# Kernel tuning notes

Hardware: AMD Instinct MI355X
Metric: run time of the kernel (lower is better)

Reference implementation:

```python
import jax, jax.numpy as jnp
import numpy as np

B, N, E, H, HID = 4, 2048, 1024, 16, 4096
D = E // H
EPS = 1e-5


def setup_inputs() -> dict:
    key = jax.random.key(0)
    ks = jax.random.split(key, 8)
    s = 0.02
    return {
        "x": jax.random.normal(ks[0], (B, N, E), dtype=jnp.float32),
        "Wqkv": jax.random.normal(ks[1], (3 * E, E), dtype=jnp.float32) * s,
        "bqkv": jnp.zeros((3 * E,), dtype=jnp.float32),
        "Wo": jax.random.normal(ks[2], (E, E), dtype=jnp.float32) * s,
        "bo": jnp.zeros((E,), dtype=jnp.float32),
        "ln1_g": jnp.ones((E,), dtype=jnp.float32),
        "ln1_b": jnp.zeros((E,), dtype=jnp.float32),
        "W1": jax.random.normal(ks[3], (HID, E), dtype=jnp.float32) * s,
        "bf1": jnp.zeros((HID,), dtype=jnp.float32),
        "W2": jax.random.normal(ks[4], (E, HID), dtype=jnp.float32) * s,
        "bf2": jnp.zeros((E,), dtype=jnp.float32),
        "ln2_g": jnp.ones((E,), dtype=jnp.float32),
        "ln2_b": jnp.zeros((E,), dtype=jnp.float32),
    }


def _layernorm(x, g, b):
    m = jnp.mean(x, axis=-1, keepdims=True)
    v = jnp.mean(jnp.square(x - m), axis=-1, keepdims=True)
    return (x - m) * jax.lax.rsqrt(v + EPS) * g + b


def reference(x, Wqkv, bqkv, Wo, bo, ln1_g, ln1_b, W1, bf1, W2, bf2, ln2_g, ln2_b):
    Bx, Nx, Ex = x.shape
    # --- MultiHeadSelfAttention (faithful to original, including its einsum-label quirk) ---
    qkv = x @ Wqkv.T + bqkv                                   # (B,N,3E)
    qkv = qkv.reshape(Bx, Nx, 3, H, D).transpose(2, 0, 3, 1, 4)  # (3,B,H,N,D)
    q, k, v = qkv[0], qkv[1], qkv[2]                          # each (B,H,N,D)
    # original torch labels: q/k interpreted as (n,q,h,d) -> energy (B,N,H,H)
    energy = jnp.einsum('nqhd,nkhd->nhqk', q, k)
    attention = jax.nn.softmax(energy / (Ex ** 0.5), axis=-1)  # softmax over heads axis
    out = jnp.einsum('nhql,nlhd->nqhd', attention, v).reshape(Bx, Nx, Ex)
    attn_out = out @ Wo.T + bo
    # --- residual + LN1 ---
    h = _layernorm(x + attn_out, ln1_g, ln1_b)
    # --- FFN (dropout is identity in eval) ---
    f = jax.nn.gelu(h @ W1.T + bf1, approximate=False) @ W2.T + bf2
    # --- residual + LN2 ---
    return _layernorm(h + f, ln2_g, ln2_b)
```

## Files before the change

### kernel.cpp

```cpp
#include <hip/hip_runtime.h>
#include <hip/hip_bf16.h>
#include <math.h>

typedef __hip_bfloat16 bf16;
typedef __bf16 bf8v __attribute__((ext_vector_type(8)));
typedef float f4v __attribute__((ext_vector_type(4)));

__device__ inline float gelu_act(float v) {
    return 0.5f * v * (1.f + erff(v * 0.70710678118654752f));
}

__device__ inline void gld16(const void* g, void* l) {
    __builtin_amdgcn_global_load_lds(
        (__attribute__((address_space(1))) void*)g,
        (__attribute__((address_space(3))) void*)l, 16, 0, 0);
}

__global__ __launch_bounds__(256)
void cast_f2b(const float* __restrict__ X, bf16* __restrict__ Y, long n)
{
    const long i = ((long)blockIdx.x * 256 + threadIdx.x) * 4;
    if (i + 3 < n) {
        const float4 v = *(const float4*)(X + i);
        Y[i + 0] = __float2bfloat16(v.x);
        Y[i + 1] = __float2bfloat16(v.y);
        Y[i + 2] = __float2bfloat16(v.z);
        Y[i + 3] = __float2bfloat16(v.w);
    }
}

template<int EPI, bool HASRES, typename CT, int KL, int KR>
__global__ __launch_bounds__(256, 4)
void gemm128(const bf16* __restrict__ A, const bf16* __restrict__ W,
             const float* __restrict__ bias, const float* __restrict__ Rr,
             CT* __restrict__ C, int N)
{
    extern __shared__ __align__(16) unsigned short lds[];
    constexpr int NT   = KL / 32;
    constexpr int SLOT = 8192;

    const int o     = blockIdx.y * gridDim.x + blockIdx.x;
    const int local = o >> 3;
    const int bm  = (o & 7) * 8 + (local & 7);
    const int bn  = local >> 3;
    const long row0 = (long)bm * 128;
    const long col0 = (long)bn * 128;
    const long koff = (long)blockIdx.z * KL;

    const int tid  = threadIdx.x;
    const int lane = tid & 63;
    const int wave = tid >> 6;
    const int wm = wave >> 1;
    const int wn = wave & 1;
    const int fr = lane & 15;
    const int q4 = (lane >> 4) * 4;
    const int ksw = (((lane >> 4) ^ ((lane >> 1) & 3)) << 3);

    const int srow = tid >> 2;
    const int csrc = (tid & 3) ^ ((srow >> 1) & 3);
    const unsigned short* gA = (const unsigned short*)A + (row0 + srow) * (long)KR + koff + csrc * 8;
    const unsigned short* gB = (const unsigned short*)W + (col0 + srow) * (long)KR + koff + csrc * 8;
    const int woff = wave * 512;

    auto stage = [&](int t) {
        const long k0 = (long)t * 32;
        unsigned short* sl = lds + (t & 1) * SLOT + woff;
        gld16(gA + k0,                  sl);
        gld16(gA + 64 * (long)KR + k0,  sl + 2048);
        gld16(gB + k0,                  sl + 4096);
        gld16(gB + 64 * (long)KR + k0,  sl + 6144);
    };

    f4v acc[4][4];
#pragma unroll
    for (int i = 0; i < 4; ++i)
#pragma unroll
        for (int j = 0; j < 4; ++j) acc[i][j] = {0.f, 0.f, 0.f, 0.f};

    stage(0);
    __syncthreads();

#pragma unroll 2
    for (int t = 0; t < NT; ++t) {
        if (t + 1 < NT) stage(t + 1);

        const unsigned short* sA = lds + (t & 1) * SLOT;
        const unsigned short* sB = sA + 4096;

        bf8v afrag[4], bfrag[4];
#pragma unroll
        for (int x = 0; x < 4; ++x) {
            afrag[x] = *(const bf8v*)&sA[(wm * 64 + x * 16 + fr) * 32 + ksw];
            bfrag[x] = *(const bf8v*)&sB[(wn * 64 + x * 16 + fr) * 32 + ksw];
        }
#pragma unroll
        for (int mi = 0; mi < 4; ++mi)
#pragma unroll
            for (int ni = 0; ni < 4; ++ni)
                acc[mi][ni] = __builtin_amdgcn_mfma_f32_16x16x32_bf16(
                    afrag[mi], bfrag[ni], acc[mi][ni], 0, 0, 0);

        __syncthreads();
    }

    if constexpr (EPI == 2) {
        const bool addb = (blockIdx.z == 0);
#pragma unroll
        for (int ni = 0; ni < 4; ++ni) {
            const long n = col0 + wn * 64 + ni * 16 + fr;
            const float bvv = addb ? bias[n] : 0.f;
#pragma unroll
            for (int mi = 0; mi < 4; ++mi) {
                const long mb = row0 + wm * 64 + mi * 16 + q4;
#pragma unroll
                for (int r = 0; r < 4; ++r)
                    atomicAdd((float*)&C[(mb + r) * (long)N + n], acc[mi][ni][r] + bvv);
            }
        }
        return;
    }

    constexpr int STR = 132;
    float* eb = (float*)lds;
    const int lcol  = (tid & 31) * 4;
    const long nbase = col0 + lcol;
    const float4 b4 = *(const float4*)&bias[nbase];
    const float bb[4] = {b4.x, b4.y, b4.z, b4.w};

#pragma unroll
    for (int h = 0; h < 2; ++h) {
        if (h) __syncthreads();
        if (wm == h) {
#pragma unroll
            for (int mi = 0; mi < 4; ++mi)
#pragma unroll
                for (int ni = 0; ni < 4; ++ni)
#pragma unroll
                    for (int r = 0; r < 4; ++r)
                        eb[(mi * 16 + q4 + r) * STR + wn * 64 + ni * 16 + fr] = acc[mi][ni][r];
        }
        __syncthreads();
#pragma unroll
        for (int i = 0; i < 8; ++i) {
            const int  rh = i * 8 + (tid >> 5);
            const long gr = row0 + h * 64 + rh;
            const f4v v = *(const f4v*)&eb[rh * STR + lcol];
            float ov[4];
#pragma unroll
            for (int c = 0; c < 4; ++c) ov[c] = v[c] + bb[c];
            if (HASRES) {
                const float4 r4 = *(const float4*)&Rr[gr * (long)N + nbase];
                const float ra[4] = {r4.x, r4.y, r4.z, r4.w};
#pragma unroll
                for (int c = 0; c < 4; ++c) ov[c] += ra[c];
            }
            if (EPI == 1) {
#pragma unroll
                for (int c = 0; c < 4; ++c) ov[c] = gelu_act(ov[c]);
            }
            if constexpr (sizeof(CT) == 2) {
                ushort4 s;
                bf16* sp = (bf16*)&s;
#pragma unroll
                for (int c = 0; c < 4; ++c) sp[c] = __float2bfloat16(ov[c]);
                *(ushort4*)&C[gr * (long)N + nbase] = s;
            } else {
                *(float4*)&C[gr * (long)N + nbase] = make_float4(ov[0], ov[1], ov[2], ov[3]);
            }
        }
    }
}

__global__ __launch_bounds__(256)
void attn_kernel(const bf16* __restrict__ qkv, bf16* __restrict__ scr)
{
    __shared__ float sb[4][3392];
    const int tid = threadIdx.x;
    const int wave = tid >> 6, lane = tid & 63;
    const int m = blockIdx.x * 4 + wave;

    float* q = sb[wave];
    float* k = q + 1040;
    float* v = k + 1040;
    float* a = v + 1040;

    const bf16* rowp = qkv + (size_t)m * 3072;
    for (int i = lane; i < 1024; i += 64) {
        int hh = i >> 6, dd = i & 63;
        q[hh * 65 + dd] = __bfloat162float(rowp[i]);
        k[hh * 65 + dd] = __bfloat162float(rowp[1024 + i]);
        v[hh * 65 + dd] = __bfloat162float(rowp[2048 + i]);
    }
    __syncthreads();

    const int h1 = lane & 15, qd = lane >> 4;
    float e[4];
#pragma unroll
    for (int j = 0; j < 4; ++j) {
        const float* qr = q + h1 * 65;
        const float* kr = k + (qd * 4 + j) * 65;
        float s0 = 0.f;
        for (int d = 0; d < 64; ++d) s0 += qr[d] * kr[d];
        e[j] = s0 * 0.03125f;
    }
    float mx = fmaxf(fmaxf(e[0], e[1]), fmaxf(e[2], e[3]));
    mx = fmaxf(mx, __shfl_xor(mx, 16, 64));
    mx = fmaxf(mx, __shfl_xor(mx, 32, 64));
    float p[4], ps = 0.f;
#pragma unroll
    for (int j = 0; j < 4; ++j) { p[j] = expf(e[j] - mx); ps += p[j]; }
    ps += __shfl_xor(ps, 16, 64);
    ps += __shfl_xor(ps, 32, 64);
    const float inv = 1.f / ps;
#pragma unroll
    for (int j = 0; j < 4; ++j) a[h1 * 17 + qd * 4 + j] = p[j] * inv;
    __syncthreads();

    const int h = lane & 15, dg = lane >> 4;
    float arow[16];
#pragma unroll
    for (int l2 = 0; l2 < 16; ++l2) arow[l2] = a[h * 17 + l2];
    const int b = m >> 11, j = m & 2047;
    bf16* op = scr + (((size_t)b * 2048 + h * 128 + (j >> 4)) * 1024 + (j & 15) * 64);
    for (int t = 0; t < 16; ++t) {
        const int d = dg * 16 + t;
        float o = 0.f;
#pragma unroll
        for (int l2 = 0; l2 < 16; ++l2) o += arow[l2] * v[l2 * 65 + d];
        op[d] = __float2bfloat16(o);
    }
}

__global__ __launch_bounds__(256)
void ln_kernel(const float* __restrict__ X, const float* __restrict__ G,
               const float* __restrict__ Bt, float* __restrict__ Y32,
               bf16* __restrict__ Yb)
{
    __shared__ float rs[4], rq[4];
    const int tid = threadIdx.x;
    const long row = blockIdx.x;
    const float* xp = X + row * 1024;
    float x[4];
#pragma unroll
    for (int i = 0; i < 4; ++i) x[i] = xp[tid + 256 * i];

    float s = x[0] + x[1] + x[2] + x[3];
#pragma unroll
    for (int off = 32; off; off >>= 1) s += __shfl_down(s, off, 64);
    if ((tid & 63) == 0) rs[tid >> 6] = s;
    __syncthreads();
    const float mean = (rs[0] + rs[1] + rs[2] + rs[3]) * (1.f / 1024.f);

    float qv = 0.f;
#pragma unroll
    for (int i = 0; i < 4; ++i) { float d = x[i] - mean; qv += d * d; }
#pragma unroll
    for (int off = 32; off; off >>= 1) qv += __shfl_down(qv, off, 64);
    if ((tid & 63) == 0) rq[tid >> 6] = qv;
    __syncthreads();
    const float var = (rq[0] + rq[1] + rq[2] + rq[3]) * (1.f / 1024.f);
    const float rstd = rsqrtf(var + 1e-5f);

#pragma unroll
    for (int i = 0; i < 4; ++i) {
        const int e = tid + 256 * i;
        const float yv = (x[i] - mean) * rstd * G[e] + Bt[e];
        Y32[row * 1024 + e] = yv;
        if (Yb) Yb[row * 1024 + e] = __float2bfloat16(yv);
    }
}

extern "C" void kernel_launch(void* const* d_in, const int* in_sizes, int n_in,
                              void* d_out, int out_size, void* d_ws, size_t ws_size,
                              hipStream_t stream)
{
    (void)in_sizes; (void)n_in; (void)out_size;
    const float* x    = (const float*)d_in[0];
    const float* Wqkv = (const float*)d_in[1];
    const float* bqkv = (const float*)d_in[2];
    const float* Wo   = (const float*)d_in[3];
    const float* bo   = (const float*)d_in[4];
    const float* g1   = (const float*)d_in[5];
    const float* b1   = (const float*)d_in[6];
    const float* W1   = (const float*)d_in[7];
    const float* bf1  = (const float*)d_in[8];
    const float* W2   = (const float*)d_in[9];
    const float* bf2  = (const float*)d_in[10];
    const float* g2   = (const float*)d_in[11];
    const float* b2   = (const float*)d_in[12];
    float* out = (float*)d_out;

    if (ws_size < 125829120ULL) return;

    char* ws = (char*)d_ws;
    bf16* qkv   = (bf16*)(ws + 0);
    float* t    = (float*)(ws + 0);
    bf16* u     = (bf16*)(ws + 0);
    bf16* Wqkvb = (bf16*)(ws + 67108864);
    bf16* Wob   = (bf16*)(ws + 73400320);
    bf16* W1b   = (bf16*)(ws + 75497472);
    bf16* W2b   = (bf16*)(ws + 83886080);
    bf16* xb    = (bf16*)(ws + 92274688);
    bf16* scr   = (bf16*)(ws + 92274688);
    bf16* hb    = (bf16*)(ws + 109051904);
    float* h    = out;

    constexpr unsigned LDS_128 = 33792;
    constexpr unsigned LDS_SPK = 32768;

    cast_f2b<<<8192, 256, 0, stream>>>(x,    xb,    8388608);
    cast_f2b<<<3072, 256, 0, stream>>>(Wqkv, Wqkvb, 3145728);
    cast_f2b<<<1024, 256, 0, stream>>>(Wo,   Wob,   1048576);
    cast_f2b<<<4096, 256, 0, stream>>>(W1,   W1b,   4194304);
    cast_f2b<<<4096, 256, 0, stream>>>(W2,   W2b,   4194304);

    gemm128<0, false, bf16, 1024, 1024><<<dim3(64, 24), 256, LDS_128, stream>>>(xb, Wqkvb, bqkv, nullptr, qkv, 3072);
    attn_kernel<<<2048, 256, 0, stream>>>(qkv, scr);
    gemm128<0, true, float, 1024, 1024><<<dim3(64, 8), 256, LDS_128, stream>>>(scr, Wob, bo, x, t, 1024);
    ln_kernel<<<8192, 256, 0, stream>>>(t, g1, b1, h, hb);
    gemm128<1, false, bf16, 1024, 1024><<<dim3(64, 32), 256, LDS_128, stream>>>(hb, W1b, bf1, nullptr, u, 4096);
    gemm128<2, false, float, 2048, 4096><<<dim3(64, 8, 2), 256, LDS_SPK, stream>>>(u, W2b, bf2, nullptr, out, 1024);
    ln_kernel<<<8192, 256, 0, stream>>>(out, g2, b2, out, nullptr);
}
```

Before: 493.9 us.

## Fuse weight casts, vectorize attention I/O, drop split-K atomics in FFN2

Merges the five fp32-to-bf16 cast launches into one kernel that writes packed 4-element bf16 stores. The attention kernel now loads q/k/v rows with 16-byte vector loads and writes its output with 16-byte vector stores instead of scalar bf16 accesses. The second FFN GEMM becomes a single full-K GEMM whose epilogue adds the residual h, in place of a two-way split-K with per-element float atomicAdd. This removes atomic traffic and redundant launches, but halves the block count of the largest GEMM, which lowers parallelism, and the residual is read from the same buffer the result is written to.

```diff
diff --git a/kernel.cpp b/kernel.cpp
--- a/kernel.cpp
+++ b/kernel.cpp
@@ -5,9 +5,18 @@
 typedef __hip_bfloat16 bf16;
 typedef __bf16 bf8v __attribute__((ext_vector_type(8)));
 typedef float f4v __attribute__((ext_vector_type(4)));
+typedef unsigned short u16x8 __attribute__((ext_vector_type(8)));
+typedef unsigned short u16x4 __attribute__((ext_vector_type(4)));
 
 __device__ inline float gelu_act(float v) {
     return 0.5f * v * (1.f + erff(v * 0.70710678118654752f));
+}
+__device__ inline float b2f(unsigned short u) {
+    return __uint_as_float((unsigned)u << 16);
+}
+__device__ inline unsigned short f2b(float f) {
+    bf16 b = __float2bfloat16(f);
+    return *reinterpret_cast<unsigned short*>(&b);
 }
 
 __device__ inline void gld16(const void* g, void* l) {
@@ -17,16 +26,24 @@
 }
 
 __global__ __launch_bounds__(256)
-void cast_f2b(const float* __restrict__ X, bf16* __restrict__ Y, long n)
-{
-    const long i = ((long)blockIdx.x * 256 + threadIdx.x) * 4;
-    if (i + 3 < n) {
-        const float4 v = *(const float4*)(X + i);
-        Y[i + 0] = __float2bfloat16(v.x);
-        Y[i + 1] = __float2bfloat16(v.y);
-        Y[i + 2] = __float2bfloat16(v.z);
-        Y[i + 3] = __float2bfloat16(v.w);
-    }
+void cast_all(const float* __restrict__ x, const float* __restrict__ Wqkv,
+              const float* __restrict__ Wo, const float* __restrict__ W1,
+              const float* __restrict__ W2, bf16* __restrict__ xb,
+              bf16* __restrict__ Wqkvb, bf16* __restrict__ Wob,
+              bf16* __restrict__ W1b, bf16* __restrict__ W2b)
+{
+    const int b = blockIdx.x;
+    const float* src; bf16* dst; long off;
+    if (b < 8192)       { src = x;    dst = xb;    off = b; }
+    else if (b < 11264) { src = Wqkv; dst = Wqkvb; off = b - 8192; }
+    else if (b < 12288) { src = Wo;   dst = Wob;   off = b - 11264; }
+    else if (b < 16384) { src = W1;   dst = W1b;   off = b - 12288; }
+    else                { src = W2;   dst = W2b;   off = b - 16384; }
+    const long i = (off * 256 + threadIdx.x) * 4;
+    const float4 v = *(const float4*)(src + i);
+    u16x4 s;
+    s[0] = f2b(v.x); s[1] = f2b(v.y); s[2] = f2b(v.z); s[3] = f2b(v.w);
+    *(u16x4*)((unsigned short*)dst + i) = s;
 }
 
 template<int EPI, bool HASRES, typename CT, int KL, int KR>
@@ -103,23 +120,6 @@
         __syncthreads();
     }
 
-    if constexpr (EPI == 2) {
-        const bool addb = (blockIdx.z == 0);
-#pragma unroll
-        for (int ni = 0; ni < 4; ++ni) {
-            const long n = col0 + wn * 64 + ni * 16 + fr;
-            const float bvv = addb ? bias[n] : 0.f;
-#pragma unroll
-            for (int mi = 0; mi < 4; ++mi) {
-                const long mb = row0 + wm * 64 + mi * 16 + q4;
-#pragma unroll
-                for (int r = 0; r < 4; ++r)
-                    atomicAdd((float*)&C[(mb + r) * (long)N + n], acc[mi][ni][r] + bvv);
-            }
-        }
-        return;
-    }
-
     constexpr int STR = 132;
     float* eb = (float*)lds;
     const int lcol  = (tid & 31) * 4;
@@ -184,12 +184,24 @@
     float* v = k + 1040;
     float* a = v + 1040;
 
-    const bf16* rowp = qkv + (size_t)m * 3072;
-    for (int i = lane; i < 1024; i += 64) {
-        int hh = i >> 6, dd = i & 63;
-        q[hh * 65 + dd] = __bfloat162float(rowp[i]);
-        k[hh * 65 + dd] = __bfloat162float(rowp[1024 + i]);
-        v[hh * 65 + dd] = __bfloat162float(rowp[2048 + i]);
+    {
+        const unsigned short* rp = (const unsigned short*)(qkv + (size_t)m * 3072) + lane * 16;
+        const int hh = lane >> 2, dd = (lane & 3) * 16;
+        const u16x8 a0 = *(const u16x8*)(rp);
+        const u16x8 a1 = *(const u16x8*)(rp + 8);
+        const u16x8 b0 = *(const u16x8*)(rp + 1024);
+        const u16x8 b1 = *(const u16x8*)(rp + 1032);
+        const u16x8 c0 = *(const u16x8*)(rp + 2048);
+        const u16x8 c1 = *(const u16x8*)(rp + 2056);
+        float* qdst = q + hh * 65 + dd;
+        float* kdst = k + hh * 65 + dd;
+        float* vdst = v + hh * 65 + dd;
+#pragma unroll
+        for (int j = 0; j < 8; ++j) {
+            qdst[j] = b2f(a0[j]); qdst[8 + j] = b2f(a1[j]);
+            kdst[j] = b2f(b0[j]); kdst[8 + j] = b2f(b1[j]);
+            vdst[j] = b2f(c0[j]); vdst[8 + j] = b2f(c1[j]);
+        }
     }
     __syncthreads();
 
@@ -222,13 +234,20 @@
     for (int l2 = 0; l2 < 16; ++l2) arow[l2] = a[h * 17 + l2];
     const int b = m >> 11, j = m & 2047;
     bf16* op = scr + (((size_t)b * 2048 + h * 128 + (j >> 4)) * 1024 + (j & 15) * 64);
+
+    float ov[16];
+#pragma unroll
     for (int t = 0; t < 16; ++t) {
-        const int d = dg * 16 + t;
         float o = 0.f;
 #pragma unroll
-        for (int l2 = 0; l2 < 16; ++l2) o += arow[l2] * v[l2 * 65 + d];
-        op[d] = __float2bfloat16(o);
-    }
+        for (int l2 = 0; l2 < 16; ++l2) o += arow[l2] * v[l2 * 65 + dg * 16 + t];
+        ov[t] = o;
+    }
+    u16x8 s0, s1;
+#pragma unroll
+    for (int jj = 0; jj < 8; ++jj) { s0[jj] = f2b(ov[jj]); s1[jj] = f2b(ov[8 + jj]); }
+    *(u16x8*)((unsigned short*)op + dg * 16)     = s0;
+    *(u16x8*)((unsigned short*)op + dg * 16 + 8) = s1;
 }
 
 __global__ __launch_bounds__(256)
@@ -306,19 +325,14 @@
     float* h    = out;
 
     constexpr unsigned LDS_128 = 33792;
-    constexpr unsigned LDS_SPK = 32768;
-
-    cast_f2b<<<8192, 256, 0, stream>>>(x,    xb,    8388608);
-    cast_f2b<<<3072, 256, 0, stream>>>(Wqkv, Wqkvb, 3145728);
-    cast_f2b<<<1024, 256, 0, stream>>>(Wo,   Wob,   1048576);
-    cast_f2b<<<4096, 256, 0, stream>>>(W1,   W1b,   4194304);
-    cast_f2b<<<4096, 256, 0, stream>>>(W2,   W2b,   4194304);
+
+    cast_all<<<20480, 256, 0, stream>>>(x, Wqkv, Wo, W1, W2, xb, Wqkvb, Wob, W1b, W2b);
 
     gemm128<0, false, bf16, 1024, 1024><<<dim3(64, 24), 256, LDS_128, stream>>>(xb, Wqkvb, bqkv, nullptr, qkv, 3072);
     attn_kernel<<<2048, 256, 0, stream>>>(qkv, scr);
     gemm128<0, true, float, 1024, 1024><<<dim3(64, 8), 256, LDS_128, stream>>>(scr, Wob, bo, x, t, 1024);
     ln_kernel<<<8192, 256, 0, stream>>>(t, g1, b1, h, hb);
     gemm128<1, false, bf16, 1024, 1024><<<dim3(64, 32), 256, LDS_128, stream>>>(hb, W1b, bf1, nullptr, u, 4096);
-    gemm128<2, false, float, 2048, 4096><<<dim3(64, 8, 2), 256, LDS_SPK, stream>>>(u, W2b, bf2, nullptr, out, 1024);
+    gemm128<0, true, float, 4096, 4096><<<dim3(64, 8), 256, LDS_128, stream>>>(u, W2b, bf2, h, out, 1024);
     ln_kernel<<<8192, 256, 0, stream>>>(out, g2, b2, out, nullptr);
 }
```

After: 454.8 us. -7.9%, faster.
